# Performance work log

Hardware: AMD Instinct MI355X
Metric: run time of the kernel (lower is better)

The kernel has to match this reference:

```python
import jax, jax.numpy as jnp
import numpy as np

B, N, D, K = 32, 4096, 128, 512
NPB = 2048          # unique tail nodes per batch (>= K so topk branch is taken)
M = B * NPB         # total unique tail nodes
E = B * N           # total edges
NUM_ENT = 10000


def setup_inputs() -> dict:
    key = jax.random.key(0)
    ks = jax.random.split(key, 18)
    f = lambda k, s: jax.random.normal(k, s, dtype=jnp.float32)
    inp = {
        "q_head": f(ks[0], (B, D)),
        "q_rel": f(ks[1], (B, D)),
        "q_time": f(ks[2], (B, D)),
        "r_neighbor": f(ks[3], (B, N, D)),
        "t_neighbor": f(ks[4], (B, N, D)),
        "time_neighbor": f(ks[5], (B, N, D)),
        "hidden": f(ks[6], (E, D)),
        "tail_emd": jnp.zeros((M, D), jnp.float32),  # scatter out-buffer
    }
    # tail_index: each edge of batch b scatters into that batch's node slab
    local = jax.random.randint(ks[7], (B, N), 0, NPB)
    inp["tail_index"] = (local + jnp.arange(B)[:, None] * NPB).reshape(E).astype(jnp.int32)
    # tail_nodes: [M,3] = (batch id, tail entity, time)
    batch_col = jnp.repeat(jnp.arange(B), NPB)
    tail_col = jax.random.randint(ks[8], (M,), 0, NUM_ENT)
    time_col = jax.random.randint(ks[9], (M,), 0, 365)
    inp["tail_nodes"] = jnp.stack([batch_col, tail_col, time_col], axis=-1).astype(jnp.int32)
    # linear-layer params (torch nn.Linear-style scaling)
    s3, s1 = 1.0 / np.sqrt(3 * D), 1.0 / np.sqrt(D)
    inp["W_q"] = f(ks[10], (3 * D, D)) * s3
    inp["b_q"] = jnp.zeros((D,), jnp.float32)
    inp["W_a"] = f(ks[11], (3 * D, D)) * s3
    inp["b_a"] = jnp.zeros((D,), jnp.float32)
    inp["W_att"] = f(ks[12], (3 * D, 1)) * s3
    inp["b_att"] = jnp.zeros((1,), jnp.float32)
    inp["W_rule"] = f(ks[13], (D, 1)) * s1
    inp["b_rule"] = jnp.zeros((1,), jnp.float32)
    inp["W_out"] = f(ks[14], (D, D)) * s1
    inp["b_out"] = jnp.zeros((D,), jnp.float32)
    return inp


def reference(q_head, q_rel, q_time, r_neighbor, t_neighbor, time_neighbor,
              hidden, tail_emd, tail_index, tail_nodes,
              W_q, b_q, W_a, b_a, W_att, b_att, W_rule, b_rule, W_out, b_out):
    # act = identity (module default). reduce = 'sum'.
    # raw message per edge: [E, D]
    message = (q_head[:, None, :] + r_neighbor + time_neighbor).reshape(E, D)
    # query / neighbor projections
    query = jnp.concatenate([q_head, q_rel, q_time], axis=-1) @ W_q + b_q      # [B, D]
    neigh = jnp.concatenate([r_neighbor, t_neighbor, time_neighbor], -1) @ W_a + b_a  # [B, N, D]
    q = query[:, None, :]
    qa = jnp.concatenate([q * neigh, q - neigh, q + neigh], axis=-1)           # [B, N, 3D]
    att1 = jax.nn.sigmoid(qa @ W_att + b_att).reshape(E, 1)
    att2 = jax.nn.sigmoid(hidden @ W_rule + b_rule)                            # [E, 1]
    att = (att1 + att2) * 0.5
    msg = att * message
    # scatter-sum aggregation over unique tail nodes
    seg = lambda v: jax.ops.segment_sum(v, tail_index, num_segments=M)
    tail_agg = tail_emd + seg(msg)            # scatter(..., out=tail_emd)
    new_hidden = seg(hidden)                  # [M, D]
    agg_att = seg(att[:, 0])                  # [M]
    # per-batch top-k over aggregated attention (each batch has NPB >= K nodes)
    nodes_batch = tail_nodes[:, 0]
    scores = jnp.where(nodes_batch[None, :] == jnp.arange(B)[:, None],
                       agg_att[None, :], -jnp.inf)                             # [B, M]
    _, idx = jax.lax.top_k(scores, K)                                          # [B, K] global node ids
    new_nodes = jnp.stack([tail_nodes[:, 1][idx], tail_nodes[:, 2][idx]], -1)  # [B, K, 2]
    emd = tail_agg[idx]                                                        # [B, K, D]
    hid = new_hidden[idx]                                                      # [B, K, D]
    out_emd = emd @ W_out + b_out                                              # act=identity
    return new_nodes, out_emd, hid
```

## Files before the change

kernel.cpp:

```cpp
#include <hip/hip_runtime.h>
#include <math.h>

#define B 32
#define N 4096
#define D 128
#define KTOP 512
#define NPB 2048
#define MSEG (B * NPB)
#define E (B * N)
#define MAXC 32
#define K7ROWS 16

__global__ __launch_bounds__(384) void k0_precompute(
    const float* __restrict__ qh, const float* __restrict__ qr,
    const float* __restrict__ qt, const float* __restrict__ Wq,
    const float* __restrict__ bq, const float* __restrict__ Wa,
    const float* __restrict__ ba, const float* __restrict__ Watt,
    const float* __restrict__ batt, float* __restrict__ vf,
    float* __restrict__ c2f) {
  int b = blockIdx.x;
  int tid = threadIdx.x;
  int d = tid & 127;
  int g = tid >> 7;
  __shared__ double part[3][128];
  __shared__ double u[128];
  __shared__ double red[128];
  const float* xs = (g == 0 ? qh : (g == 1 ? qr : qt)) + b * 128;
  const float* Wg = Wq + g * 128 * 128;
  double a0 = 0, a1 = 0, a2 = 0, a3 = 0;
#pragma unroll 4
  for (int i = 0; i < 128; i += 4) {
    a0 += (double)xs[i] * (double)Wg[i * 128 + d];
    a1 += (double)xs[i + 1] * (double)Wg[(i + 1) * 128 + d];
    a2 += (double)xs[i + 2] * (double)Wg[(i + 2) * 128 + d];
    a3 += (double)xs[i + 3] * (double)Wg[(i + 3) * 128 + d];
  }
  part[g][d] = (a0 + a1) + (a2 + a3);
  __syncthreads();
  if (g == 0) {
    double acc = (double)bq[d] + part[0][d] + part[1][d] + part[2][d];
    double w1 = (double)Watt[d], w2 = (double)Watt[128 + d],
           w3 = (double)Watt[256 + d];
    double ud = acc * w1 - w2 + w3;
    u[d] = ud;
    red[d] = acc * (w2 + w3) + (double)ba[d] * ud;
  }
  __syncthreads();
  for (int s = 64; s > 0; s >>= 1) {
    if (tid < s) red[tid] += red[tid + s];
    __syncthreads();
  }
  if (tid == 0) c2f[b] = (float)(red[0] + (double)batt[0]);
  {
    double v0 = 0, v1 = 0, v2 = 0, v3 = 0;
    const float* Wr = Wa + tid * 128;
#pragma unroll 4
    for (int dd = 0; dd < 128; dd += 4) {
      v0 += (double)Wr[dd] * u[dd];
      v1 += (double)Wr[dd + 1] * u[dd + 1];
      v2 += (double)Wr[dd + 2] * u[dd + 2];
      v3 += (double)Wr[dd + 3] * u[dd + 3];
    }
    vf[b * 384 + tid] = (float)((v0 + v1) + (v2 + v3));
  }
}

__global__ __launch_bounds__(256) void k1_att(
    const float* __restrict__ r, const float* __restrict__ t,
    const float* __restrict__ tm, const float* __restrict__ hidden,
    const float* __restrict__ Wrule, const float* __restrict__ brule,
    const float* __restrict__ vf, const float* __restrict__ c2f,
    const int* __restrict__ tidx, float* __restrict__ attw,
    double* __restrict__ aggd) {
  int tid = threadIdx.x;
  int h = tid >> 5;
  int l = tid & 31;
  int base = blockIdx.x * 64;
  int b = base >> 12;
  const float4* vb = (const float4*)(vf + b * 384);
  float4 v0 = vb[l];
  float4 v1 = vb[32 + l];
  float4 v2 = vb[64 + l];
  float4 wr = ((const float4*)Wrule)[l];
  float c2 = c2f[b];
  float br = brule[0];
  int mseg[8];
#pragma unroll
  for (int i = 0; i < 8; ++i) mseg[i] = tidx[base + i * 8 + h];
  float4 ra[4], ta[4], ma[4], ha[4];
  size_t lo = (size_t)(l * 4);
#pragma unroll
  for (int i = 0; i < 4; ++i) {
    size_t eo = (size_t)(base + i * 8 + h) * 128 + lo;
    ra[i] = *(const float4*)(r + eo);
    ta[i] = *(const float4*)(t + eo);
    ma[i] = *(const float4*)(tm + eo);
    ha[i] = *(const float4*)(hidden + eo);
  }
#pragma unroll
  for (int i = 0; i < 8; ++i) {
    float4 A = ra[i & 3], T = ta[i & 3], M = ma[i & 3], H = ha[i & 3];
    if (i < 4) {
      size_t eo = (size_t)(base + (i + 4) * 8 + h) * 128 + lo;
      ra[i & 3] = *(const float4*)(r + eo);
      ta[i & 3] = *(const float4*)(t + eo);
      ma[i & 3] = *(const float4*)(tm + eo);
      ha[i & 3] = *(const float4*)(hidden + eo);
    }
    float p1 = A.x * v0.x + A.y * v0.y + A.z * v0.z + A.w * v0.w;
    p1 += T.x * v1.x + T.y * v1.y + T.z * v1.z + T.w * v1.w;
    p1 += M.x * v2.x + M.y * v2.y + M.z * v2.z + M.w * v2.w;
    float p2 = H.x * wr.x + H.y * wr.y + H.z * wr.z + H.w * wr.w;
#pragma unroll
    for (int off = 16; off > 0; off >>= 1) {
      p1 += __shfl_xor(p1, off);
      p2 += __shfl_xor(p2, off);
    }
    if (l == 0) {
      int e = base + i * 8 + h;
      float a1 = 1.0f / (1.0f + expf(-(p1 + c2)));
      float a2 = 1.0f / (1.0f + expf(-(p2 + br)));
      float a = 0.5f * (a1 + a2);
      attw[e] = a;
      atomicAdd(&aggd[mseg[i]], (double)a);
    }
  }
}

__global__ __launch_bounds__(256) void kb_build(const int* __restrict__ tidx,
                                                int* __restrict__ counts,
                                                int* __restrict__ lists) {
  int e = blockIdx.x * 256 + threadIdx.x;
  int m = tidx[e];
  int pos = atomicAdd(&counts[m], 1);
  if (pos < MAXC) lists[m * MAXC + pos] = e;
}

__global__ __launch_bounds__(256) void k6_topk(
    const double* __restrict__ aggd, const int* __restrict__ tail_nodes,
    float* __restrict__ out_nodes, int* __restrict__ idxw) {
  __shared__ double sv[2048];
  int b = blockIdx.x >> 3;
  int chunk = blockIdx.x & 7;
  int tid = threadIdx.x;
  for (int s = tid; s < 2048; s += 256) sv[s] = aggd[b * 2048 + s];
  __syncthreads();
  int i = chunk * 256 + tid;
  double vi = sv[i];
  int rank = 0;
#pragma unroll 8
  for (int j = 0; j < 2048; ++j) {
    double vj = sv[j];
    rank += (vj > vi) || (vj == vi && j < i);
  }
  if (rank < KTOP) {
    int gm = b * 2048 + i;
    int p = b * KTOP + rank;
    out_nodes[p * 2 + 0] = (float)tail_nodes[gm * 3 + 1];
    out_nodes[p * 2 + 1] = (float)tail_nodes[gm * 3 + 2];
    idxw[p] = gm;
  }
}

__global__ __launch_bounds__(256) void k7_out(
    const float* __restrict__ tail_emd, const float* __restrict__ r,
    const float* __restrict__ tm, const float* __restrict__ hidden,
    const float* __restrict__ qh, const float* __restrict__ attw,
    const int* __restrict__ counts, const int* __restrict__ lists,
    const float* __restrict__ Wout, const float* __restrict__ bout,
    const int* __restrict__ idxw, float* __restrict__ out_emd,
    float* __restrict__ out_hid) {
  __shared__ float es[K7ROWS][128];
  int tid = threadIdx.x;
  int sub = tid >> 7, d = tid & 127;
  int base = blockIdx.x * K7ROWS;
  for (int j = 0; j < K7ROWS; j += 2) {
    int row = base + j + sub;
    int m = idxw[row];
    int b = m >> 11;
    int cnt = counts[m];
    if (cnt > MAXC) cnt = MAXC;
    float accT = tail_emd[(size_t)m * 128 + d];
    float accH = 0.f;
    float qhd = qh[b * 128 + d];
    for (int jj = 0; jj < cnt; ++jj) {
      int e = lists[m * MAXC + jj];
      float a = attw[e];
      size_t eo = (size_t)e * 128 + d;
      accT += a * (qhd + r[eo] + tm[eo]);
      accH += hidden[eo];
    }
    es[j + sub][d] = accT;
    out_hid[(size_t)row * 128 + d] = accH;
  }
  __syncthreads();
  int cg = tid & 31;
  int rg = tid >> 5;
  float4 bo = *(const float4*)(bout + cg * 4);
  float acc0x = bo.x, acc0y = bo.y, acc0z = bo.z, acc0w = bo.w;
  float acc1x = bo.x, acc1y = bo.y, acc1z = bo.z, acc1w = bo.w;
#pragma unroll 4
  for (int i = 0; i < 128; ++i) {
    float4 w = *(const float4*)(Wout + i * 128 + cg * 4);
    float e0 = es[rg * 2 + 0][i];
    float e1 = es[rg * 2 + 1][i];
    acc0x += e0 * w.x; acc0y += e0 * w.y; acc0z += e0 * w.z; acc0w += e0 * w.w;
    acc1x += e1 * w.x; acc1y += e1 * w.y; acc1z += e1 * w.z; acc1w += e1 * w.w;
  }
  size_t r0 = (size_t)(base + rg * 2) * 128 + cg * 4;
  *(float4*)(out_emd + r0) = make_float4(acc0x, acc0y, acc0z, acc0w);
  *(float4*)(out_emd + r0 + 128) = make_float4(acc1x, acc1y, acc1z, acc1w);
}

extern "C" void kernel_launch(void* const* d_in, const int* in_sizes, int n_in,
                              void* d_out, int out_size, void* d_ws,
                              size_t ws_size, hipStream_t stream) {
  const float* q_head = (const float*)d_in[0];
  const float* q_rel = (const float*)d_in[1];
  const float* q_time = (const float*)d_in[2];
  const float* r_nb = (const float*)d_in[3];
  const float* t_nb = (const float*)d_in[4];
  const float* tm_nb = (const float*)d_in[5];
  const float* hidden = (const float*)d_in[6];
  const float* tail_emd = (const float*)d_in[7];
  const int* tail_index = (const int*)d_in[8];
  const int* tail_nodes = (const int*)d_in[9];
  const float* W_q = (const float*)d_in[10];
  const float* b_q = (const float*)d_in[11];
  const float* W_a = (const float*)d_in[12];
  const float* b_a = (const float*)d_in[13];
  const float* W_att = (const float*)d_in[14];
  const float* b_att = (const float*)d_in[15];
  const float* W_rule = (const float*)d_in[16];
  const float* b_rule = (const float*)d_in[17];
  const float* W_out = (const float*)d_in[18];
  const float* b_out = (const float*)d_in[19];

  char* ws = (char*)d_ws;
  float* vf = (float*)(ws + 0);
  float* c2f = (float*)(ws + 49152);
  float* attw = (float*)(ws + 49280);
  int* counts = (int*)(ws + 573568);
  double* aggd = (double*)(ws + 835712);
  int* lists = (int*)(ws + 1360000);
  int* idxw = (int*)(ws + 9748608);

  float* out_nodes = (float*)d_out;
  float* out_emd = (float*)d_out + (size_t)B * KTOP * 2;
  float* out_hid = out_emd + (size_t)B * KTOP * 128;

  hipMemsetAsync(counts, 0, MSEG * sizeof(int) + MSEG * sizeof(double), stream);
  k0_precompute<<<B, 384, 0, stream>>>(q_head, q_rel, q_time, W_q, b_q, W_a,
                                       b_a, W_att, b_att, vf, c2f);
  k1_att<<<E / 64, 256, 0, stream>>>(r_nb, t_nb, tm_nb, hidden, W_rule, b_rule,
                                     vf, c2f, tail_index, attw, aggd);
  kb_build<<<E / 256, 256, 0, stream>>>(tail_index, counts, lists);
  k6_topk<<<B * 8, 256, 0, stream>>>(aggd, tail_nodes, out_nodes, idxw);
  k7_out<<<(B * KTOP) / K7ROWS, 256, 0, stream>>>(tail_emd, r_nb, tm_nb,
                                                  hidden, q_head, attw, counts,
                                                  lists, W_out, b_out, idxw,
                                                  out_emd, out_hid);
}
```

Baseline: 444.1 us.

## Fuse zeroing and list building into precompute and attention kernels, prefetch edge lists

Removes the memset by zeroing counts and aggregate buffers inside k0, and folds the bucket-list build into k1_att so each warp's lanes 0-7 do the atomics for their edges. k1 switches from 4-deep to double-buffered register prefetch with an occupancy hint. k7 preloads row ids, counts and the first four list entries per row so the gathers are issued earlier. This saves two launches and the separate pass over the index array, at the cost of more register pressure in k7 and a change in prefetch depth in k1.

```diff
diff --git a/kernel.cpp b/kernel.cpp
--- a/kernel.cpp
+++ b/kernel.cpp
@@ -17,9 +17,18 @@
     const float* __restrict__ bq, const float* __restrict__ Wa,
     const float* __restrict__ ba, const float* __restrict__ Watt,
     const float* __restrict__ batt, float* __restrict__ vf,
-    float* __restrict__ c2f) {
+    float* __restrict__ c2f, int* __restrict__ counts,
+    double* __restrict__ aggd) {
   int b = blockIdx.x;
   int tid = threadIdx.x;
+  {
+    int t = b * 384 + tid;
+    float4 z = make_float4(0.f, 0.f, 0.f, 0.f);
+    float4* cz = (float4*)counts;
+    float4* az = (float4*)aggd;
+    for (int i = t; i < 16384; i += 12288) cz[i] = z;
+    for (int i = t; i < 32768; i += 12288) az[i] = z;
+  }
   int d = tid & 127;
   int g = tid >> 7;
   __shared__ double part[3][128];
@@ -65,13 +74,14 @@
   }
 }
 
-__global__ __launch_bounds__(256) void k1_att(
+__global__ __launch_bounds__(256, 8) void k1_att(
     const float* __restrict__ r, const float* __restrict__ t,
     const float* __restrict__ tm, const float* __restrict__ hidden,
     const float* __restrict__ Wrule, const float* __restrict__ brule,
     const float* __restrict__ vf, const float* __restrict__ c2f,
     const int* __restrict__ tidx, float* __restrict__ attw,
-    double* __restrict__ aggd) {
+    double* __restrict__ aggd, int* __restrict__ counts,
+    int* __restrict__ lists) {
   int tid = threadIdx.x;
   int h = tid >> 5;
   int l = tid & 31;
@@ -84,29 +94,30 @@
   float4 wr = ((const float4*)Wrule)[l];
   float c2 = c2f[b];
   float br = brule[0];
-  int mseg[8];
-#pragma unroll
-  for (int i = 0; i < 8; ++i) mseg[i] = tidx[base + i * 8 + h];
-  float4 ra[4], ta[4], ma[4], ha[4];
-  size_t lo = (size_t)(l * 4);
-#pragma unroll
-  for (int i = 0; i < 4; ++i) {
-    size_t eo = (size_t)(base + i * 8 + h) * 128 + lo;
-    ra[i] = *(const float4*)(r + eo);
-    ta[i] = *(const float4*)(t + eo);
-    ma[i] = *(const float4*)(tm + eo);
-    ha[i] = *(const float4*)(hidden + eo);
+  int myseg = 0;
+  if (l < 8) myseg = tidx[base + l * 8 + h];
+  float mya = 0.f;
+  unsigned lo = (unsigned)(l * 4);
+  float4 ra[2], ta[2], ma[2], ha[2];
+  {
+    unsigned eo = ((unsigned)(base + h) << 7) + lo;
+    ra[0] = *(const float4*)(r + eo);
+    ta[0] = *(const float4*)(t + eo);
+    ma[0] = *(const float4*)(tm + eo);
+    ha[0] = *(const float4*)(hidden + eo);
   }
 #pragma unroll
   for (int i = 0; i < 8; ++i) {
-    float4 A = ra[i & 3], T = ta[i & 3], M = ma[i & 3], H = ha[i & 3];
-    if (i < 4) {
-      size_t eo = (size_t)(base + (i + 4) * 8 + h) * 128 + lo;
-      ra[i & 3] = *(const float4*)(r + eo);
-      ta[i & 3] = *(const float4*)(t + eo);
-      ma[i & 3] = *(const float4*)(tm + eo);
-      ha[i & 3] = *(const float4*)(hidden + eo);
-    }
+    const int cur = i & 1;
+    if (i < 7) {
+      const int nxt = cur ^ 1;
+      unsigned eo = ((unsigned)(base + (i + 1) * 8 + h) << 7) + lo;
+      ra[nxt] = *(const float4*)(r + eo);
+      ta[nxt] = *(const float4*)(t + eo);
+      ma[nxt] = *(const float4*)(tm + eo);
+      ha[nxt] = *(const float4*)(hidden + eo);
+    }
+    float4 A = ra[cur], T = ta[cur], M = ma[cur], H = ha[cur];
     float p1 = A.x * v0.x + A.y * v0.y + A.z * v0.z + A.w * v0.w;
     p1 += T.x * v1.x + T.y * v1.y + T.z * v1.z + T.w * v1.w;
     p1 += M.x * v2.x + M.y * v2.y + M.z * v2.z + M.w * v2.w;
@@ -116,24 +127,19 @@
       p1 += __shfl_xor(p1, off);
       p2 += __shfl_xor(p2, off);
     }
-    if (l == 0) {
-      int e = base + i * 8 + h;
+    if (l == i) {
       float a1 = 1.0f / (1.0f + expf(-(p1 + c2)));
       float a2 = 1.0f / (1.0f + expf(-(p2 + br)));
-      float a = 0.5f * (a1 + a2);
-      attw[e] = a;
-      atomicAdd(&aggd[mseg[i]], (double)a);
-    }
-  }
-}
-
-__global__ __launch_bounds__(256) void kb_build(const int* __restrict__ tidx,
-                                                int* __restrict__ counts,
-                                                int* __restrict__ lists) {
-  int e = blockIdx.x * 256 + threadIdx.x;
-  int m = tidx[e];
-  int pos = atomicAdd(&counts[m], 1);
-  if (pos < MAXC) lists[m * MAXC + pos] = e;
+      mya = 0.5f * (a1 + a2);
+    }
+  }
+  if (l < 8) {
+    int e = base + l * 8 + h;
+    attw[e] = mya;
+    atomicAdd(&aggd[myseg], (double)mya);
+    int pos = atomicAdd(&counts[myseg], 1);
+    if (pos < MAXC) lists[myseg * MAXC + pos] = e;
+  }
 }
 
 __global__ __launch_bounds__(256) void k6_topk(
@@ -174,24 +180,57 @@
   int tid = threadIdx.x;
   int sub = tid >> 7, d = tid & 127;
   int base = blockIdx.x * K7ROWS;
-  for (int j = 0; j < K7ROWS; j += 2) {
-    int row = base + j + sub;
-    int m = idxw[row];
-    int b = m >> 11;
-    int cnt = counts[m];
-    if (cnt > MAXC) cnt = MAXC;
+  int mrow[8], crow[8];
+#pragma unroll
+  for (int jj = 0; jj < 8; ++jj) mrow[jj] = idxw[base + jj * 2 + sub];
+#pragma unroll
+  for (int jj = 0; jj < 8; ++jj) crow[jj] = counts[mrow[jj]];
+  int4 el[8];
+#pragma unroll
+  for (int jj = 0; jj < 8; ++jj)
+    el[jj] = *(const int4*)(lists + (size_t)mrow[jj] * MAXC);
+#pragma unroll
+  for (int jj = 0; jj < 8; ++jj) {
+    int m = mrow[jj];
+    int bb = m >> 11;
+    int cnt = crow[jj] > MAXC ? MAXC : crow[jj];
     float accT = tail_emd[(size_t)m * 128 + d];
     float accH = 0.f;
-    float qhd = qh[b * 128 + d];
-    for (int jj = 0; jj < cnt; ++jj) {
-      int e = lists[m * MAXC + jj];
+    float qhd = qh[bb * 128 + d];
+    int e0 = el[jj].x, e1 = el[jj].y, e2 = el[jj].z, e3 = el[jj].w;
+    if (cnt > 0) {
+      float a = attw[e0];
+      size_t eo = (size_t)e0 * 128 + d;
+      accT += a * (qhd + r[eo] + tm[eo]);
+      accH += hidden[eo];
+    }
+    if (cnt > 1) {
+      float a = attw[e1];
+      size_t eo = (size_t)e1 * 128 + d;
+      accT += a * (qhd + r[eo] + tm[eo]);
+      accH += hidden[eo];
+    }
+    if (cnt > 2) {
+      float a = attw[e2];
+      size_t eo = (size_t)e2 * 128 + d;
+      accT += a * (qhd + r[eo] + tm[eo]);
+      accH += hidden[eo];
+    }
+    if (cnt > 3) {
+      float a = attw[e3];
+      size_t eo = (size_t)e3 * 128 + d;
+      accT += a * (qhd + r[eo] + tm[eo]);
+      accH += hidden[eo];
+    }
+    for (int k = 4; k < cnt; ++k) {
+      int e = lists[(size_t)m * MAXC + k];
       float a = attw[e];
       size_t eo = (size_t)e * 128 + d;
       accT += a * (qhd + r[eo] + tm[eo]);
       accH += hidden[eo];
     }
-    es[j + sub][d] = accT;
-    out_hid[(size_t)row * 128 + d] = accH;
+    es[jj * 2 + sub][d] = accT;
+    out_hid[(size_t)(base + jj * 2 + sub) * 128 + d] = accH;
   }
   __syncthreads();
   int cg = tid & 31;
@@ -249,12 +288,12 @@
   float* out_emd = (float*)d_out + (size_t)B * KTOP * 2;
   float* out_hid = out_emd + (size_t)B * KTOP * 128;
 
-  hipMemsetAsync(counts, 0, MSEG * sizeof(int) + MSEG * sizeof(double), stream);
   k0_precompute<<<B, 384, 0, stream>>>(q_head, q_rel, q_time, W_q, b_q, W_a,
-                                       b_a, W_att, b_att, vf, c2f);
+                                       b_a, W_att, b_att, vf, c2f, counts,
+                                       aggd);
   k1_att<<<E / 64, 256, 0, stream>>>(r_nb, t_nb, tm_nb, hidden, W_rule, b_rule,
-                                     vf, c2f, tail_index, attw, aggd);
-  kb_build<<<E / 256, 256, 0, stream>>>(tail_index, counts, lists);
+                                     vf, c2f, tail_index, attw, aggd, counts,
+                                     lists);
   k6_topk<<<B * 8, 256, 0, stream>>>(aggd, tail_nodes, out_nodes, idxw);
   k7_out<<<(B * KTOP) / K7ROWS, 256, 0, stream>>>(tail_emd, r_nb, tm_nb,
                                                   hidden, q_head, attw, counts,
```

Result: faster. 431.7 us (-2.8%).
